# Kernel optimization log

Measured on AMD Instinct MI355X. Metric: run time of the kernel, lower is better.

Reference implementation:

```python
import math
import jax, jax.numpy as jnp
import numpy as np
from jax import lax

D = 384; NHEAD = 12; NLAYERS = 4; H = 128; WIN = (128, 24); NS = (1, 10); B = 256; CONV_C = 128

def _interleave(s, c):
    # [s0,c0,s1,c1,...] along last dim (matches 0::2=sin, 1::2=cos)
    return jnp.stack([s, c], axis=-1).reshape(s.shape[:-1] + (s.shape[-1] * 2,))

def _pos_encoding():
    d3 = D // 3
    div = jnp.exp(jnp.arange(0, d3, 2, dtype=jnp.float32) * (-math.log(10000.0) / d3))
    coord = jnp.arange(H, dtype=jnp.float32) - H // 2
    pe1d = _interleave(jnp.sin(coord[:, None] * div), jnp.cos(coord[:, None] * div))  # (H, d3)
    pe_y = jnp.broadcast_to(pe1d[:, None, :], (H, H, d3))
    pe_x = jnp.broadcast_to(pe1d[None, :, :], (H, H, d3))
    ws = jnp.array(WIN, dtype=jnp.float32)
    pe_w = _interleave(jnp.sin(ws[:, None] * div), jnp.cos(ws[:, None] * div))  # (2, d3)
    pe_yx = jnp.concatenate([pe_y, pe_x], axis=-1)  # (H, H, 2*d3)
    pe = jnp.concatenate([
        jnp.broadcast_to(pe_yx[:, :, None, :], (H, H, len(WIN), 2 * d3)),
        jnp.broadcast_to(pe_w[None, None, :, :], (H, H, len(WIN), d3))], axis=-1)
    return pe  # (H, H, 2, D)

def _windows(img3, pos, ws):
    # img3: (B,3,H,W); pos: (n,2) int. Crop [y1:y2, x1:x2] then zero-pad bottom/right to ws x ws.
    hw = ws // 2
    y = jnp.clip(pos[:, 0], 0, H - 1); x = jnp.clip(pos[:, 1], 0, H - 1)
    y1 = jnp.maximum(0, y - hw); y2 = jnp.minimum(H, y + hw)
    x1 = jnp.maximum(0, x - hw); x2 = jnp.minimum(H, x + hw)
    r = jnp.arange(ws)
    rows = y1[:, None] + r; cols = x1[:, None] + r  # (n, ws)
    mask = (rows < y2[:, None])[:, :, None] & (cols < x2[:, None])[:, None, :]  # (n, ws, ws)
    win = img3[:, :, jnp.clip(rows, 0, H - 1)[:, :, None], jnp.clip(cols, 0, H - 1)[:, None, :]]  # (B,3,n,ws,ws)
    win = jnp.where(mask[None, None], win, 0.0)
    return jnp.transpose(win, (0, 2, 1, 3, 4))  # (B, n, 3, ws, ws)

def _layer_norm(x, g, b):
    m = x.mean(-1, keepdims=True)
    v = ((x - m) ** 2).mean(-1, keepdims=True)
    return (x - m) / jnp.sqrt(v + 1e-5) * g + b

def _encoder_layer(x, Wqkv, bqkv, Wo, bo, g1, b1, g2, b2, W1, bf1, W2, bf2):
    Bsz, S, _ = x.shape
    dh = D // NHEAD
    qkv = x @ Wqkv.T + bqkv
    q, k, v = jnp.split(qkv, 3, axis=-1)
    heads = lambda t: t.reshape(Bsz, S, NHEAD, dh).transpose(0, 2, 1, 3)
    q, k, v = heads(q), heads(k), heads(v)
    att = jax.nn.softmax(jnp.einsum('bhqd,bhkd->bhqk', q, k) / math.sqrt(dh), axis=-1)
    o = jnp.einsum('bhqk,bhkd->bhqd', att, v).transpose(0, 2, 1, 3).reshape(Bsz, S, D)
    x = _layer_norm(x + o @ Wo.T + bo, g1, b1)
    ff = jax.nn.relu(x @ W1.T + bf1) @ W2.T + bf2
    return _layer_norm(x + ff, g2, b2)

def _normalize(v):
    return v / jnp.maximum(jnp.linalg.norm(v, axis=1, keepdims=True), 1e-12)

def _forward(pos0, pos1, rgb_image, conv_w, conv_b, ext_w, ext_b, proj_w, proj_b,
             Wqkv, bqkv, Wo, bo, ln1g, ln1b, ln2g, ln2b, Wff1, bff1, Wff2, bff2,
             rw1, rb1, rw2, rb2, uw1, ub1, uw2, ub2):
    Bsz = rgb_image.shape[0]
    img3 = rgb_image[:, :3]
    win0 = _windows(img3, pos0, WIN[0]).reshape(Bsz * NS[0], 3, WIN[0], WIN[0])
    win1 = _windows(img3, pos1, WIN[1])  # (B, 10, 3, 24, 24)
    h = lax.conv_general_dilated(win0, conv_w, (4, 4), 'SAME')
    h = jax.nn.relu(h + conv_b[None, :, None, None])
    f0 = (h.mean((2, 3)) @ ext_w.T + ext_b).reshape(Bsz, NS[0], D)
    f1 = win1.reshape(Bsz, NS[1], -1) @ proj_w.T + proj_b  # (B,10,D)
    feats = jnp.concatenate([f0, f1], axis=1)  # (B, 11, D)
    pe = _pos_encoding()
    pp = jnp.concatenate([
        jnp.concatenate([pos0, jnp.zeros((NS[0], 1), pos0.dtype)], axis=1),
        jnp.concatenate([pos1, jnp.ones((NS[1], 1), pos1.dtype)], axis=1)], axis=0)  # (11, 3)
    pf = pe[pp[:, 0], pp[:, 1], pp[:, 2]]  # (11, D)
    x = feats + pf[None]
    for i in range(NLAYERS):
        x = _encoder_layer(x, Wqkv[i], bqkv[i], Wo[i], bo[i], ln1g[i], ln1b[i],
                           ln2g[i], ln2b[i], Wff1[i], bff1[i], Wff2[i], bff2[i])
    m = x.mean(axis=1)
    r = jax.nn.relu(m @ rw1.T + rb1) @ rw2.T + rb2
    r1, r2 = r[:, :3], r[:, 3:]
    r2 = r2 - jnp.sum(r1 * r2, axis=1, keepdims=True) * r1
    r3 = jnp.cross(r1, r2)
    R = jnp.concatenate([_normalize(r1), _normalize(r2), _normalize(r3)], axis=1)
    uv = jax.nn.sigmoid(jax.nn.relu(m @ uw1.T + ub1) @ uw2.T + ub2)
    return (uv, R)

def setup_inputs():
    key = jax.random.key(0)
    ks = iter(jax.random.split(key, 40))
    w = lambda *s: jax.random.normal(next(ks), s, jnp.float32) * 0.02
    return dict(
        rgb_image=jax.random.uniform(next(ks), (B, 4, H, H), jnp.float32),
        pos0=jax.random.randint(next(ks), (NS[0], 2), 0, H).astype(jnp.int32),
        pos1=jax.random.randint(next(ks), (NS[1], 2), 0, H).astype(jnp.int32),
        conv_w=w(CONV_C, 3, 7, 7), conv_b=jnp.zeros((CONV_C,), jnp.float32),
        ext_w=w(D, CONV_C), ext_b=jnp.zeros((D,), jnp.float32),
        proj_w=w(D, WIN[1] * WIN[1] * 3), proj_b=jnp.zeros((D,), jnp.float32),
        Wqkv=w(NLAYERS, 3 * D, D), bqkv=jnp.zeros((NLAYERS, 3 * D), jnp.float32),
        Wo=w(NLAYERS, D, D), bo=jnp.zeros((NLAYERS, D), jnp.float32),
        ln1g=jnp.ones((NLAYERS, D), jnp.float32), ln1b=jnp.zeros((NLAYERS, D), jnp.float32),
        ln2g=jnp.ones((NLAYERS, D), jnp.float32), ln2b=jnp.zeros((NLAYERS, D), jnp.float32),
        Wff1=w(NLAYERS, 2048, D), bff1=jnp.zeros((NLAYERS, 2048), jnp.float32),
        Wff2=w(NLAYERS, D, 2048), bff2=jnp.zeros((NLAYERS, D), jnp.float32),
        rw1=w(D, D), rb1=jnp.zeros((D,), jnp.float32),
        rw2=w(6, D), rb2=jnp.zeros((6,), jnp.float32),
        uw1=w(D, D), ub1=jnp.zeros((D,), jnp.float32),
        uw2=w(2, D), ub2=jnp.zeros((2,), jnp.float32),
    )

def reference(rgb_image, pos0, pos1, conv_w, conv_b, ext_w, ext_b, proj_w, proj_b,
              Wqkv, bqkv, Wo, bo, ln1g, ln1b, ln2g, ln2b, Wff1, bff1, Wff2, bff2,
              rw1, rb1, rw2, rb2, uw1, ub1, uw2, ub2):
    return _forward(pos0, pos1, rgb_image, conv_w, conv_b, ext_w, ext_b, proj_w, proj_b,
                    Wqkv, bqkv, Wo, bo, ln1g, ln1b, ln2g, ln2b, Wff1, bff1, Wff2, bff2,
                    rw1, rb1, rw2, rb2, uw1, ub1, uw2, ub2)
```

## Files before the change

kernel.cpp:

```cpp
#include <hip/hip_runtime.h>
#include <hip/hip_bf16.h>

#define B_ 256
#define S_ 11
#define D_ 384
#define NHEAD_ 12

typedef const float* bfp;
typedef __attribute__((ext_vector_type(8))) __bf16 bf16x8;
typedef __attribute__((ext_vector_type(4))) float f32x4;

__device__ __forceinline__ bf16x8 ld8_b64(const __bf16* p) {
    union { unsigned long long q[2]; bf16x8 v; } u;
    u.q[0] = *reinterpret_cast<const unsigned long long*>(p);
    u.q[1] = *reinterpret_cast<const unsigned long long*>(p + 4);
    return u.v;
}

__device__ __forceinline__ void gl16(const __bf16* g, __bf16* l) {
    __builtin_amdgcn_global_load_lds(
        (const __attribute__((address_space(1))) void*)g,
        (__attribute__((address_space(3))) void*)l, 16, 0, 0);
}

__global__ void prep_k(const float* __restrict__ proj_w, const float* __restrict__ Wqkv,
                       const float* __restrict__ Wo, const float* __restrict__ Wff1,
                       const float* __restrict__ Wff2,
                       __bf16* __restrict__ projWb, __bf16* __restrict__ WqkvB,
                       __bf16* __restrict__ WoB, __bf16* __restrict__ Wff1B,
                       __bf16* __restrict__ Wff2B,
                       const float* __restrict__ cw, __bf16* __restrict__ wpad,
                       const int* __restrict__ pos0, const int* __restrict__ pos1,
                       float* __restrict__ pf,
                       const float* __restrict__ rw1, const float* __restrict__ uw1,
                       float* __restrict__ rw1T, float* __restrict__ uw1T,
                       float* __restrict__ f0pre,
                       bfp __restrict__ img, __bf16* __restrict__ pimg)
{
    int i = blockIdx.x * 256 + threadIdx.x;
    if (i < 2328576) {
        const float* s; __bf16* d; int off;
        if      (i < 165888)  { s = proj_w; d = projWb; off = i; }
        else if (i < 608256)  { s = Wqkv;   d = WqkvB;  off = i - 165888; }
        else if (i < 755712)  { s = Wo;     d = WoB;    off = i - 608256; }
        else if (i < 1542144) { s = Wff1;   d = Wff1B;  off = i - 755712; }
        else                  { s = Wff2;   d = Wff2B;  off = i - 1542144; }
        float4 v = reinterpret_cast<const float4*>(s)[off];
        union { __bf16 h[4]; unsigned long long u; } p;
        p.h[0] = (__bf16)v.x; p.h[1] = (__bf16)v.y;
        p.h[2] = (__bf16)v.z; p.h[3] = (__bf16)v.w;
        reinterpret_cast<unsigned long long*>(d)[off] = p.u;
        return;
    }
    if (i < 2331648) {
        int e = i - 2328576;
        int r = e >> 5, g = e & 31;
        if (g >= 24) return;
        union { __bf16 h[8]; uint4 u; } w;
        #pragma unroll
        for (int kx = 0; kx < 8; ++kx) {
            float v = 0.f;
            if (g < 21 && kx < 7) v = cw[(size_t)r * 147 + g * 7 + kx];
            w.h[kx] = (__bf16)v;
        }
        *reinterpret_cast<uint4*>(&wpad[(size_t)r * 192 + g * 8]) = w.u;
        return;
    }
    if (i < 2332032) {
        int dd0 = i - 2331648;
        const float c1 = -logf(10000.f) / 128.f;
        for (int ss = 0; ss < 11; ++ss) {
            int py, px, pw;
            if (ss == 0) { py = pos0[0]; px = pos0[1]; pw = 0; }
            else { py = pos1[(ss - 1) * 2]; px = pos1[(ss - 1) * 2 + 1]; pw = 1; }
            float coordv; int dd = dd0;
            if (dd0 < 128) coordv = (float)(py - 64);
            else if (dd0 < 256) { coordv = (float)(px - 64); dd = dd0 - 128; }
            else { coordv = (pw == 0) ? 128.f : 24.f; dd = dd0 - 256; }
            int ii = dd >> 1;
            float div = expf((float)(2 * ii) * c1);
            float ang = coordv * div;
            pf[ss * 384 + dd0] = (dd & 1) ? cosf(ang) : sinf(ang);
        }
        return;
    }
    if (i < 2626944) {
        int e = i - 2332032;
        int which = e >= 147456;
        int t = which ? e - 147456 : e;
        int k = t / 384, dd = t - k * 384;
        if (which) uw1T[k * 384 + dd] = uw1[(size_t)dd * 384 + k];
        else       rw1T[k * 384 + dd] = rw1[(size_t)dd * 384 + k];
        return;
    }
    if (i < 2659712) {
        f0pre[i - 2626944] = 0.f;
        return;
    }
    if (i < 4484480) {
        int e = i - 2659712;
        int col8 = e % 18, t = e / 18;
        int row = t % 132; t /= 132;
        int ch = t % 3; int b = t / 3;
        int y = min(max(pos0[0], 0), 127), x = min(max(pos0[1], 0), 127);
        int y1 = max(0, y - 64), y2 = min(128, y + 64);
        int x1 = max(0, x - 64), x2 = min(128, x + 64);
        int iy = y1 + row - 1;
        bool rok = (row >= 1) && (iy < y2);
        const float* src = img + ((size_t)(b * 4 + ch) * 128 + iy) * 128;
        union { __bf16 h[8]; uint4 u; } p;
        #pragma unroll
        for (int k = 0; k < 8; ++k) {
            int cc = col8 * 8 + k;
            int ix = x1 + cc - 1;
            float v = 0.f;
            if (rok && cc >= 1 && ix < x2) v = src[ix];
            p.h[k] = (__bf16)v;
        }
        *reinterpret_cast<uint4*>(&pimg[((size_t)(b * 3 + ch) * 132 + row) * 144 + col8 * 8]) = p.u;
        return;
    }
}

__global__ void win1_k(bfp __restrict__ img, const int* __restrict__ pos1,
                       __bf16* __restrict__ w1)
{
    int i = blockIdx.x * 256 + threadIdx.x;
    if (i >= B_ * 10 * 1728) return;
    int cc = i % 24, r = (i / 24) % 24, c = (i / 576) % 3, s = (i / 1728) % 10, b = i / 17280;
    int y = min(max(pos1[s * 2], 0), 127), x = min(max(pos1[s * 2 + 1], 0), 127);
    int y1 = max(0, y - 12), y2 = min(128, y + 12);
    int x1 = max(0, x - 12), x2 = min(128, x + 12);
    float v = 0.f;
    if ((y1 + r) < y2 && (x1 + cc) < x2)
        v = img[((size_t)(b * 4 + c) * 128 + (y1 + r)) * 128 + (x1 + cc)];
    w1[i] = (__bf16)v;
}

__global__ __launch_bounds__(256) void gemm_bb_k(
    const __bf16* __restrict__ A, const __bf16* __restrict__ W,
    const float* __restrict__ bias, const float* __restrict__ resid,
    void* __restrict__ C_, int M, int N, int K, int mode, int outBf16, int kChunk)
{
    __shared__ __align__(16) __bf16 AsF[2][8192];
    __shared__ __align__(16) __bf16 WsF[2][4096];
    const int tid = threadIdx.x;
    const int bm = blockIdx.y * 128, bn = blockIdx.x * 64;
    const int z = blockIdx.z;
    int kStart = 0, kEnd = K;
    if (kChunk) { kStart = z * kChunk; kEnd = min(K, kStart + kChunk); }
    const int lane = tid & 63, wv = tid >> 6;
    const int wrA = (wv >> 1) * 64, wcW = (wv & 1) * 32;
    const int lr = lane & 15, lk = lane >> 4;
    size_t gaoff[4], gwoff[2];
    #pragma unroll
    for (int k = 0; k < 4; ++k) {
        int c = tid + k * 256; int r = c >> 3; int j = (c & 7) ^ (r & 7);
        gaoff[k] = (size_t)(bm + r) * K + j * 8;
    }
    #pragma unroll
    for (int k = 0; k < 2; ++k) {
        int c = tid + k * 256; int r = c >> 3; int j = (c & 7) ^ (r & 7);
        gwoff[k] = (size_t)(bn + r) * K + j * 8;
    }
    f32x4 acc[4][2] = {};

#define STAGE_(bf, kk) do {                                       \
        gl16(A + gaoff[0] + (kk), &AsF[bf][(wv << 9)]);           \
        gl16(A + gaoff[1] + (kk), &AsF[bf][2048 + (wv << 9)]);    \
        gl16(A + gaoff[2] + (kk), &AsF[bf][4096 + (wv << 9)]);    \
        gl16(A + gaoff[3] + (kk), &AsF[bf][6144 + (wv << 9)]);    \
        gl16(W + gwoff[0] + (kk), &WsF[bf][(wv << 9)]);           \
        gl16(W + gwoff[1] + (kk), &WsF[bf][2048 + (wv << 9)]);    \
    } while (0)

    STAGE_(0, kStart);
    __syncthreads();
    int cur = 0;
    for (int k0 = kStart; k0 < kEnd; k0 += 64) {
        if (k0 + 64 < kEnd) STAGE_(cur ^ 1, k0 + 64);
        const __bf16* Ab = AsF[cur];
        const __bf16* Wb = WsF[cur];
        #pragma unroll
        for (int s = 0; s < 2; ++s) {
            int j = s * 4 + lk;
            int rw0 = wcW + lr, rw1_ = wcW + 16 + lr;
            bf16x8 w0 = *reinterpret_cast<const bf16x8*>(&Wb[rw0 * 64 + ((j ^ (rw0 & 7)) << 3)]);
            bf16x8 w1 = *reinterpret_cast<const bf16x8*>(&Wb[rw1_ * 64 + ((j ^ (rw1_ & 7)) << 3)]);
            #pragma unroll
            for (int m = 0; m < 4; ++m) {
                int ra = wrA + m * 16 + lr;
                bf16x8 a = *reinterpret_cast<const bf16x8*>(&Ab[ra * 64 + ((j ^ (ra & 7)) << 3)]);
                acc[m][0] = __builtin_amdgcn_mfma_f32_16x16x32_bf16(a, w0, acc[m][0], 0, 0, 0);
                acc[m][1] = __builtin_amdgcn_mfma_f32_16x16x32_bf16(a, w1, acc[m][1], 0, 0, 0);
            }
        }
        __syncthreads();
        cur ^= 1;
    }
#undef STAGE_
    if (kChunk) {
        float* Cp = (float*)C_ + (size_t)z * M * N;
        #pragma unroll
        for (int m = 0; m < 4; ++m)
            #pragma unroll
            for (int n = 0; n < 2; ++n) {
                int col = bn + wcW + n * 16 + lr;
                #pragma unroll
                for (int i = 0; i < 4; ++i) {
                    int row = bm + wrA + m * 16 + lk * 4 + i;
                    Cp[(size_t)row * N + col] = acc[m][n][i];
                }
            }
    } else {
        #pragma unroll
        for (int m = 0; m < 4; ++m)
            #pragma unroll
            for (int n = 0; n < 2; ++n) {
                int col = bn + wcW + n * 16 + lr;
                float bcol = bias[col];
                #pragma unroll
                for (int i = 0; i < 4; ++i) {
                    int row = bm + wrA + m * 16 + lk * 4 + i;
                    float v = acc[m][n][i] + bcol;
                    if (mode == 1) v = fmaxf(v, 0.f);
                    if (mode == 2) v += resid[(size_t)row * N + col];
                    if (outBf16) ((__bf16*)C_)[(size_t)row * N + col] = (__bf16)v;
                    else         ((float*)C_)[(size_t)row * N + col] = v;
                }
            }
    }
}

__global__ __launch_bounds__(256) void gemm_bb128_k(
    const __bf16* __restrict__ A, const __bf16* __restrict__ W,
    const float* __restrict__ bias, void* __restrict__ C_,
    int M, int N, int K, int mode, int outBf16)
{
    __shared__ __align__(16) __bf16 AsF[2][8192];
    __shared__ __align__(16) __bf16 WsF[2][8192];
    const int tid = threadIdx.x;
    const int bm = blockIdx.y * 128, bn = blockIdx.x * 128;
    const int lane = tid & 63, wv = tid >> 6;
    const int wrA = (wv >> 1) * 64, wcW = (wv & 1) * 64;
    const int lr = lane & 15, lk = lane >> 4;
    size_t gaoff[4], gwoff[4];
    #pragma unroll
    for (int k = 0; k < 4; ++k) {
        int c = tid + k * 256; int r = c >> 3; int j = (c & 7) ^ (r & 7);
        gaoff[k] = (size_t)(bm + r) * K + j * 8;
        gwoff[k] = (size_t)(bn + r) * K + j * 8;
    }
    f32x4 acc[4][4] = {};

#define STAGE_(bf, kk) do {                                           \
        gl16(A + gaoff[0] + (kk), &AsF[bf][(wv << 9)]);               \
        gl16(A + gaoff[1] + (kk), &AsF[bf][2048 + (wv << 9)]);        \
        gl16(A + gaoff[2] + (kk), &AsF[bf][4096 + (wv << 9)]);        \
        gl16(A + gaoff[3] + (kk), &AsF[bf][6144 + (wv << 9)]);        \
        gl16(W + gwoff[0] + (kk), &WsF[bf][(wv << 9)]);               \
        gl16(W + gwoff[1] + (kk), &WsF[bf][2048 + (wv << 9)]);        \
        gl16(W + gwoff[2] + (kk), &WsF[bf][4096 + (wv << 9)]);        \
        gl16(W + gwoff[3] + (kk), &WsF[bf][6144 + (wv << 9)]);        \
    } while (0)

    STAGE_(0, 0);
    __syncthreads();
    int cur = 0;
    for (int k0 = 0; k0 < K; k0 += 64) {
        if (k0 + 64 < K) STAGE_(cur ^ 1, k0 + 64);
        const __bf16* Ab = AsF[cur];
        const __bf16* Wb = WsF[cur];
        #pragma unroll
        for (int s = 0; s < 2; ++s) {
            int j = s * 4 + lk;
            bf16x8 wfrag[4];
            #pragma unroll
            for (int n = 0; n < 4; ++n) {
                int rw = wcW + n * 16 + lr;
                wfrag[n] = *reinterpret_cast<const bf16x8*>(&Wb[rw * 64 + ((j ^ (rw & 7)) << 3)]);
            }
            #pragma unroll
            for (int m = 0; m < 4; ++m) {
                int ra = wrA + m * 16 + lr;
                bf16x8 a = *reinterpret_cast<const bf16x8*>(&Ab[ra * 64 + ((j ^ (ra & 7)) << 3)]);
                #pragma unroll
                for (int n = 0; n < 4; ++n)
                    acc[m][n] = __builtin_amdgcn_mfma_f32_16x16x32_bf16(a, wfrag[n], acc[m][n], 0, 0, 0);
            }
        }
        __syncthreads();
        cur ^= 1;
    }
#undef STAGE_
    #pragma unroll
    for (int m = 0; m < 4; ++m)
        #pragma unroll
        for (int n = 0; n < 4; ++n) {
            int col = bn + wcW + n * 16 + lr;
            float bcol = bias[col];
            #pragma unroll
            for (int i = 0; i < 4; ++i) {
                int row = bm + wrA + m * 16 + lk * 4 + i;
                float v = acc[m][n][i] + bcol;
                if (mode == 1) v = fmaxf(v, 0.f);
                if (outBf16) ((__bf16*)C_)[(size_t)row * N + col] = (__bf16)v;
                else         ((float*)C_)[(size_t)row * N + col] = v;
            }
        }
}

__global__ __launch_bounds__(256) void convgemm_k(
    const __bf16* __restrict__ pimg, const __bf16* __restrict__ wpad,
    bfp __restrict__ cb, float* __restrict__ f0pre)
{
    __shared__ __align__(16) __bf16 Wlds[64][200];
    __shared__ __align__(16) __bf16 P[2][4896];
    const int tid = threadIdx.x;
    const int blk = blockIdx.x;
    const int b = blk >> 3;
    const int bn = ((blk >> 2) & 1) * 64;
    const int mtg = blk & 3;
    const int lane = tid & 63, wv = tid >> 6;
    const int wr = (wv >> 1) * 32, wc = (wv & 1) * 32;
    const int lr = lane & 15, lk = lane >> 4;
    const int oyl = wr >> 5;
    const int ox0 = lr, ox1 = 16 + lr;

    size_t poff[3]; bool pval[3];
    #pragma unroll
    for (int p = 0; p < 3; ++p) {
        int c = tid + p * 256;
        pval[p] = (c < 612);
        int col8 = c % 17, rowi = c / 17;
        int r2 = rowi % 12, c3 = rowi / 12;
        poff[p] = ((size_t)(b * 3 + c3) * 132 + r2) * 144 + col8 * 8;
    }
#define STAGEP_(buf, mt) do {                                                 \
        if (pval[0]) gl16(pimg + poff[0] + (size_t)(mt) * 1152, &P[buf][(0 + (wv << 6)) * 8]);      \
        if (pval[1]) gl16(pimg + poff[1] + (size_t)(mt) * 1152, &P[buf][(256 + (wv << 6)) * 8]);    \
        if (pval[2]) gl16(pimg + poff[2] + (size_t)(mt) * 1152, &P[buf][(512 + (wv << 6)) * 8]);    \
    } while (0)

    STAGEP_(0, mtg * 4);
    for (int e = tid; e < 1536; e += 256) {
        int r = e / 24, g = e - r * 24;
        uint4 q = *reinterpret_cast<const uint4*>(&wpad[(size_t)(bn + r) * 192 + g * 8]);
        *reinterpret_cast<uint4*>(&Wlds[r][g * 8]) = q;
    }
    __syncthreads();

    float s0 = 0.f, s1 = 0.f;
    const float bc0 = cb[bn + wc + lr];
    const float bc1 = cb[bn + wc + 16 + lr];

    for (int t = 0; t < 4; ++t) {
        if (t < 3) STAGEP_((t + 1) & 1, mtg * 4 + t + 1);
        const __bf16* Pb = P[t & 1];
        f32x4 acc[2][2] = {};
        #pragma unroll
        for (int kk = 0; kk < 6; ++kk) {
            int g = kk * 4 + lk;
            int c = g / 7, ky = g - c * 7;
            if (g >= 21) { c = 0; ky = 0; }
            const __bf16* prow = &Pb[(c * 12 + oyl * 4 + ky) * 136];
            bf16x8 a0 = ld8_b64(prow + ox0 * 4);
            bf16x8 a1 = ld8_b64(prow + ox1 * 4);
            bf16x8 w0 = *reinterpret_cast<const bf16x8*>(&Wlds[wc + lr][g * 8]);
            bf16x8 w1 = *reinterpret_cast<const bf16x8*>(&Wlds[wc + 16 + lr][g * 8]);
            acc[0][0] = __builtin_amdgcn_mfma_f32_16x16x32_bf16(a0, w0, acc[0][0], 0, 0, 0);
            acc[0][1] = __builtin_amdgcn_mfma_f32_16x16x32_bf16(a0, w1, acc[0][1], 0, 0, 0);
            acc[1][0] = __builtin_amdgcn_mfma_f32_16x16x32_bf16(a1, w0, acc[1][0], 0, 0, 0);
            acc[1][1] = __builtin_amdgcn_mfma_f32_16x16x32_bf16(a1, w1, acc[1][1], 0, 0, 0);
        }
        #pragma unroll
        for (int m = 0; m < 2; ++m)
            #pragma unroll
            for (int i = 0; i < 4; ++i) {
                s0 += fmaxf(acc[m][0][i] + bc0, 0.f);
                s1 += fmaxf(acc[m][1][i] + bc1, 0.f);
            }
        __syncthreads();
    }
#undef STAGEP_
    s0 += __shfl_xor(s0, 16); s0 += __shfl_xor(s0, 32);
    s1 += __shfl_xor(s1, 16); s1 += __shfl_xor(s1, 32);
    if (lk == 0) {
        atomicAdd(&f0pre[b * 128 + bn + wc + lr],      s0 * (1.f / 1024.f));
        atomicAdd(&f0pre[b * 128 + bn + wc + 16 + lr], s1 * (1.f / 1024.f));
    }
}

__global__ void assemble_k(const float* __restrict__ f0pre, bfp __restrict__ ew,
                           bfp __restrict__ eb,
                           const float* __restrict__ p0, const float* __restrict__ p1,
                           const float* __restrict__ projb,
                           const float* __restrict__ pf, float* __restrict__ x,
                           __bf16* __restrict__ xb)
{
    int i = blockIdx.x * 256 + threadIdx.x;
    if (i >= B_ * S_ * D_) return;
    int d = i % 384, s = (i / 384) % 11, b = i / (384 * 11);
    float f;
    if (s == 0) {
        float acc = eb[d];
        const float* pre = f0pre + b * 128;
        const float* wrow = ew + (size_t)d * 128;
        #pragma unroll 4
        for (int co = 0; co < 128; ++co) acc += pre[co] * wrow[co];
        f = acc;
    } else {
        size_t o = ((size_t)(b * 10) + (s - 1)) * 384 + d;
        f = p0[o] + p1[o] + projb[d];
    }
    float v = f + pf[s * 384 + d];
    x[i] = v;
    xb[i] = (__bf16)v;
}

__global__ __launch_bounds__(256) void attn_k(const __bf16* __restrict__ qkv,
                                              __bf16* __restrict__ obuf)
{
    int b = blockIdx.x;
    __shared__ __bf16 qs[11][1160];
    __shared__ float att[12][11][11];
    const __bf16* src = qkv + (size_t)b * 11 * 1152;
    for (int c = threadIdx.x; c < 1584; c += 256) {
        int row = c / 144, col8 = c - row * 144;
        *reinterpret_cast<uint4*>(&qs[row][col8 * 8]) =
            *reinterpret_cast<const uint4*>(&src[c * 8]);
    }
    __syncthreads();
    for (int t = threadIdx.x; t < 1452; t += 256) {
        int h = t / 121, r = t - h * 121;
        int i = r / 11, j = r - i * 11;
        const __bf16* qp = &qs[i][h * 32];
        const __bf16* kp = &qs[j][384 + h * 32];
        float s = 0.f;
        #pragma unroll
        for (int d8 = 0; d8 < 4; ++d8) {
            bf16x8 qv = ld8_b64(qp + d8 * 8);
            bf16x8 kv = ld8_b64(kp + d8 * 8);
            #pragma unroll
            for (int e = 0; e < 8; ++e) s += (float)qv[e] * (float)kv[e];
        }
        att[h][i][j] = s * 0.17677669529663687f;
    }
    __syncthreads();
    for (int t = threadIdx.x; t < 132; t += 256) {
        int h = t / 11, i = t - h * 11;
        float mx = att[h][i][0];
        #pragma unroll
        for (int j = 1; j < 11; ++j) mx = fmaxf(mx, att[h][i][j]);
        float e_[11], sum = 0.f;
        #pragma unroll
        for (int j = 0; j < 11; ++j) { e_[j] = expf(att[h][i][j] - mx); sum += e_[j]; }
        float inv = 1.f / sum;
        #pragma unroll
        for (int j = 0; j < 11; ++j) att[h][i][j] = e_[j] * inv;
    }
    __syncthreads();
    for (int t = threadIdx.x; t < 4224; t += 256) {
        int i = t / 384, col = t - i * 384;
        int h = col >> 5;
        float s = 0.f;
        #pragma unroll
        for (int j = 0; j < 11; ++j) s += att[h][i][j] * (float)qs[j][768 + col];
        obuf[((size_t)b * 11 + i) * 384 + col] = (__bf16)s;
    }
}

__global__ __launch_bounds__(512) void ln_k(const float* __restrict__ parts, int nparts,
                                            const float* __restrict__ resid,
                                            const float* __restrict__ bias,
                                            bfp g, bfp be, float* __restrict__ xo,
                                            __bf16* __restrict__ xb)
{
    int row = blockIdx.x * 8 + (threadIdx.x >> 6);
    int lane = threadIdx.x & 63;
    const size_t MN = (size_t)2816 * 384;
    float v[6];
    float s = 0.f, sq = 0.f;
    #pragma unroll
    for (int j = 0; j < 6; ++j) {
        int d = lane + 64 * j;
        size_t off = (size_t)row * 384 + d;
        float t = resid[off] + bias[d];
        for (int z = 0; z < nparts; ++z) t += parts[z * MN + off];
        v[j] = t; s += t; sq += t * t;
    }
    #pragma unroll
    for (int o = 32; o >= 1; o >>= 1) { s += __shfl_xor(s, o); sq += __shfl_xor(sq, o); }
    float mean = s * (1.f / 384.f);
    float var = sq * (1.f / 384.f) - mean * mean;
    float inv = rsqrtf(var + 1e-5f);
    float* xr = xo + (size_t)row * 384;
    __bf16* xbr = xb + (size_t)row * 384;
    #pragma unroll
    for (int j = 0; j < 6; ++j) {
        int d = lane + 64 * j;
        float o = (v[j] - mean) * inv * g[d] + be[d];
        xr[d] = o;
        xbr[d] = (__bf16)o;
    }
}

__global__ __launch_bounds__(768) void headfused_k(
    const float* __restrict__ X,
    const float* __restrict__ rw1T, bfp __restrict__ rb1,
    const float* __restrict__ uw1T, bfp __restrict__ ub1,
    bfp __restrict__ rw2, bfp __restrict__ rb2, bfp __restrict__ uw2, bfp __restrict__ ub2,
    float* __restrict__ out)
{
    __shared__ float m[384], ph1[2][384], ph2[2][384], h1s[384], h2s[384];
    int b = blockIdx.x, t = threadIdx.x;
    int half = t / 384, d = t - half * 384;
    if (half == 0) {
        float s = 0.f;
        for (int si = 0; si < 11; ++si) s += X[((size_t)b * 11 + si) * 384 + d];
        m[d] = s * (1.f / 11.f);
    }
    __syncthreads();
    {
        float a1 = 0.f, a2 = 0.f;
        int k0 = half * 192;
        #pragma unroll 8
        for (int k = k0; k < k0 + 192; ++k) {
            float mk = m[k];
            a1 += mk * rw1T[k * 384 + d];
            a2 += mk * uw1T[k * 384 + d];
        }
        ph1[half][d] = a1;
        ph2[half][d] = a2;
    }
    __syncthreads();
    if (half == 0) {
        h1s[d] = fmaxf(ph1[0][d] + ph1[1][d] + rb1[d], 0.f);
        h2s[d] = fmaxf(ph2[0][d] + ph2[1][d] + ub1[d], 0.f);
    }
    __syncthreads();
    if (t < 64) {
        int lane = t;
        float acc[8] = {};
        for (int dd = lane; dd < 384; dd += 64) {
            float v1 = h1s[dd], v2 = h2s[dd];
            #pragma unroll
            for (int o = 0; o < 6; ++o) acc[o] += v1 * rw2[o * 384 + dd];
            acc[6] += v2 * uw2[dd];
            acc[7] += v2 * uw2[384 + dd];
        }
        #pragma unroll
        for (int o = 0; o < 8; ++o)
            #pragma unroll
            for (int off = 32; off >= 1; off >>= 1) acc[o] += __shfl_xor(acc[o], off);
        if (lane == 0) {
            float r[6];
            for (int o = 0; o < 6; ++o) r[o] = acc[o] + rb2[o];
            float u0 = acc[6] + ub2[0], u1 = acc[7] + ub2[1];
            float dot12 = r[0] * r[3] + r[1] * r[4] + r[2] * r[5];
            float q2x = r[3] - dot12 * r[0], q2y = r[4] - dot12 * r[1], q2z = r[5] - dot12 * r[2];
            float q3x = r[1] * q2z - r[2] * q2y;
            float q3y = r[2] * q2x - r[0] * q2z;
            float q3z = r[0] * q2y - r[1] * q2x;
            float n1 = fmaxf(sqrtf(r[0]*r[0] + r[1]*r[1] + r[2]*r[2]), 1e-12f);
            float n2 = fmaxf(sqrtf(q2x*q2x + q2y*q2y + q2z*q2z), 1e-12f);
            float n3 = fmaxf(sqrtf(q3x*q3x + q3y*q3y + q3z*q3z), 1e-12f);
            out[b * 2 + 0] = 1.f / (1.f + expf(-u0));
            out[b * 2 + 1] = 1.f / (1.f + expf(-u1));
            float* R = out + B_ * 2 + b * 9;
            R[0] = r[0] / n1; R[1] = r[1] / n1; R[2] = r[2] / n1;
            R[3] = q2x / n2;  R[4] = q2y / n2;  R[5] = q2z / n2;
            R[6] = q3x / n3;  R[7] = q3y / n3;  R[8] = q3z / n3;
        }
    }
}

extern "C" void kernel_launch(void* const* d_in, const int* in_sizes, int n_in,
                              void* d_out, int out_size, void* d_ws, size_t ws_size,
                              hipStream_t stream)
{
    bfp rgb     = (bfp)d_in[0];
    const int* pos0 = (const int*)d_in[1];
    const int* pos1 = (const int*)d_in[2];
    bfp conv_w  = (bfp)d_in[3];
    bfp conv_b  = (bfp)d_in[4];
    bfp ext_w   = (bfp)d_in[5];
    bfp ext_b   = (bfp)d_in[6];
    bfp proj_w  = (bfp)d_in[7];
    bfp proj_b  = (bfp)d_in[8];
    bfp Wqkv    = (bfp)d_in[9];
    bfp bqkv    = (bfp)d_in[10];
    bfp Wo      = (bfp)d_in[11];
    bfp bo      = (bfp)d_in[12];
    bfp ln1g    = (bfp)d_in[13];
    bfp ln1b    = (bfp)d_in[14];
    bfp ln2g    = (bfp)d_in[15];
    bfp ln2b    = (bfp)d_in[16];
    bfp Wff1    = (bfp)d_in[17];
    bfp bff1    = (bfp)d_in[18];
    bfp Wff2    = (bfp)d_in[19];
    bfp bff2    = (bfp)d_in[20];
    bfp rw1     = (bfp)d_in[21];
    bfp rb1     = (bfp)d_in[22];
    bfp rw2     = (bfp)d_in[23];
    bfp rb2     = (bfp)d_in[24];
    bfp uw1     = (bfp)d_in[25];
    bfp ub1     = (bfp)d_in[26];
    bfp uw2     = (bfp)d_in[27];
    bfp ub2     = (bfp)d_in[28];

    float* ws = (float*)d_ws;
    float*  X      = ws;
    __bf16* PIMG   = (__bf16*)(ws + 1081344);
    float*  QKV    = ws + 2162688;
    __bf16* QKVb   = (__bf16*)QKV;
    float*  PP0    = ws + 3276800;
    float*  PP1    = ws + 4259840;
    __bf16* OBUFb  = (__bf16*)(ws + 5406720);
    __bf16* FFH16  = (__bf16*)(ws + 6144000);
    __bf16* WIN1F16= FFH16;
    float*  PF     = ws + 9027584;
    float*  F0PRE  = ws + 9031808;
    __bf16* Xb     = (__bf16*)(ws + 9130112);
    __bf16* projWb = (__bf16*)(ws + 9670784);
    __bf16* WqkvB  = (__bf16*)(ws + 10002560);
    __bf16* WoB    = (__bf16*)(ws + 10887296);
    __bf16* Wff1B  = (__bf16*)(ws + 11182208);
    __bf16* Wff2B  = (__bf16*)(ws + 12755072);
    __bf16* WpadC  = (__bf16*)(ws + 14327936);
    float*  RW1T   = ws + 14340224;
    float*  UW1T   = ws + 14487680;

    prep_k<<<17518, 256, 0, stream>>>(proj_w, Wqkv, Wo, Wff1, Wff2,
                                      projWb, WqkvB, WoB, Wff1B, Wff2B,
                                      conv_w, WpadC, pos0, pos1, PF,
                                      rw1, uw1, RW1T, UW1T,
                                      F0PRE, rgb, PIMG);
    convgemm_k<<<2048, 256, 0, stream>>>(PIMG, WpadC, conv_b, F0PRE);
    win1_k<<<(B_ * 10 * 1728 + 255) / 256, 256, 0, stream>>>(rgb, pos1, WIN1F16);
    gemm_bb_k<<<dim3(6, 20, 2), 256, 0, stream>>>(WIN1F16, projWb, nullptr, nullptr,
                                                  PP0, 2560, 384, 1728, 0, 0, 896);
    assemble_k<<<(B_ * S_ * D_ + 255) / 256, 256, 0, stream>>>(
        F0PRE, ext_w, ext_b, PP0, PP1, proj_b, PF, X, Xb);

    for (int i = 0; i < 4; ++i) {
        gemm_bb_k<<<dim3(18, 22), 256, 0, stream>>>(
            Xb, WqkvB + (size_t)i * 1152 * 384, bqkv + i * 1152, nullptr, QKVb,
            2816, 1152, 384, 0, 1, 0);
        attn_k<<<B_, 256, 0, stream>>>(QKVb, OBUFb);
        gemm_bb_k<<<dim3(6, 22, 2), 256, 0, stream>>>(
            OBUFb, WoB + (size_t)i * 384 * 384, nullptr, nullptr, QKV,
            2816, 384, 384, 0, 0, 192);
        ln_k<<<352, 512, 0, stream>>>(QKV, 2, X, bo + i * 384,
                                      ln1g + i * 384, ln1b + i * 384, X, Xb);
        gemm_bb128_k<<<dim3(16, 22), 256, 0, stream>>>(
            Xb, Wff1B + (size_t)i * 2048 * 384, bff1 + i * 2048, FFH16,
            2816, 2048, 384, 1, 1);
        gemm_bb_k<<<dim3(6, 22, 2), 256, 0, stream>>>(
            FFH16, Wff2B + (size_t)i * 384 * 2048, nullptr, nullptr, QKV,
            2816, 384, 2048, 0, 0, 1024);
        ln_k<<<352, 512, 0, stream>>>(QKV, 2, X, bff2 + i * 384,
                                      ln2g + i * 384, ln2b + i * 384, X, Xb);
    }

    headfused_k<<<256, 768, 0, stream>>>(X, RW1T, rb1, UW1T, ub1,
                                         rw2, rb2, uw2, ub2, (float*)d_out);
}
```

Baseline: 432.9 us.

## Triple-buffer GEMM LDS staging with explicit vmcnt waits and single barrier

Moves the bf16 GEMM's global-to-LDS staging from double to triple buffering. Loads are issued two tiles ahead, and fine-grained s_waitcnt vmcnt(6) plus a single s_barrier per iteration replace the trailing __syncthreads. The aim is to hide global load latency and drop one barrier per k-step. In exchange, LDS use rises by half, which may lower occupancy. The wraparound staging also issues redundant loads in the last two iterations, and it assumes at least two k-tiles per chunk.

```diff
diff --git a/kernel.cpp b/kernel.cpp
--- a/kernel.cpp
+++ b/kernel.cpp
@@ -142,8 +142,8 @@
     const float* __restrict__ bias, const float* __restrict__ resid,
     void* __restrict__ C_, int M, int N, int K, int mode, int outBf16, int kChunk)
 {
-    __shared__ __align__(16) __bf16 AsF[2][8192];
-    __shared__ __align__(16) __bf16 WsF[2][4096];
+    __shared__ __align__(16) __bf16 AsF[3][8192];
+    __shared__ __align__(16) __bf16 WsF[3][4096];
     const int tid = threadIdx.x;
     const int bm = blockIdx.y * 128, bn = blockIdx.x * 64;
     const int z = blockIdx.z;
@@ -165,22 +165,30 @@
     }
     f32x4 acc[4][2] = {};
 
-#define STAGE_(bf, kk) do {                                       \
-        gl16(A + gaoff[0] + (kk), &AsF[bf][(wv << 9)]);           \
-        gl16(A + gaoff[1] + (kk), &AsF[bf][2048 + (wv << 9)]);    \
-        gl16(A + gaoff[2] + (kk), &AsF[bf][4096 + (wv << 9)]);    \
-        gl16(A + gaoff[3] + (kk), &AsF[bf][6144 + (wv << 9)]);    \
-        gl16(W + gwoff[0] + (kk), &WsF[bf][(wv << 9)]);           \
-        gl16(W + gwoff[1] + (kk), &WsF[bf][2048 + (wv << 9)]);    \
+#define STAGE3_(nb, kk) do {                                            \
+        __bf16* bA = &AsF[nb][0]; __bf16* bW = &WsF[nb][0];             \
+        gl16(A + gaoff[0] + (kk), bA + (wv << 9));                      \
+        gl16(A + gaoff[1] + (kk), bA + 2048 + (wv << 9));               \
+        gl16(A + gaoff[2] + (kk), bA + 4096 + (wv << 9));               \
+        gl16(A + gaoff[3] + (kk), bA + 6144 + (wv << 9));               \
+        gl16(W + gwoff[0] + (kk), bW + (wv << 9));                      \
+        gl16(W + gwoff[1] + (kk), bW + 2048 + (wv << 9));               \
     } while (0)
 
-    STAGE_(0, kStart);
-    __syncthreads();
+    const int nIter = (kEnd - kStart) >> 6;
+    STAGE3_(0, kStart);
+    STAGE3_(1, kStart + 64);
     int cur = 0;
-    for (int k0 = kStart; k0 < kEnd; k0 += 64) {
-        if (k0 + 64 < kEnd) STAGE_(cur ^ 1, k0 + 64);
-        const __bf16* Ab = AsF[cur];
-        const __bf16* Wb = WsF[cur];
+    for (int it = 0; it < nIter; ++it) {
+        asm volatile("s_waitcnt vmcnt(6)" ::: "memory");
+        __builtin_amdgcn_sched_barrier(0);
+        asm volatile("s_waitcnt lgkmcnt(0)" ::: "memory");
+        __builtin_amdgcn_s_barrier();
+        int nxt = it + 2; if (nxt >= nIter) nxt -= nIter;
+        int nb = cur + 2; if (nb >= 3) nb -= 3;
+        STAGE3_(nb, kStart + nxt * 64);
+        const __bf16* Ab = &AsF[cur][0];
+        const __bf16* Wb = &WsF[cur][0];
         #pragma unroll
         for (int s = 0; s < 2; ++s) {
             int j = s * 4 + lk;
@@ -195,10 +203,9 @@
                 acc[m][1] = __builtin_amdgcn_mfma_f32_16x16x32_bf16(a, w1, acc[m][1], 0, 0, 0);
             }
         }
-        __syncthreads();
-        cur ^= 1;
-    }
-#undef STAGE_
+        cur = cur + 1; if (cur == 3) cur = 0;
+    }
+#undef STAGE3_
     if (kChunk) {
         float* Cp = (float*)C_ + (size_t)z * M * N;
         #pragma unroll
```

Result: slower. 461.9 us (+6.7%).
